# Kernel tuning notes

Measured on AMD Instinct MI355X. Metric: run time of the kernel, lower is better.

The kernel has to match this reference:

```python
import jax, jax.numpy as jnp
import numpy as np

U, S, D = 4096, 8192, 32
NUM_REGIONS = 128
GA = 0.1


def setup_inputs() -> dict:
    key = jax.random.key(0)
    k1, k2, k3, k4, k5, k6 = jax.random.split(key, 6)
    user_emb = jax.random.normal(k1, (U, D), dtype=jnp.float32) * 0.01
    item_emb = jax.random.normal(k2, (S, D), dtype=jnp.float32) * 0.01
    train_mask = jax.random.randint(k3, (U, S), 0, 2, dtype=jnp.int32)
    true_qos = jax.random.normal(k4, (U, S), dtype=jnp.float32)
    us_lossweight = jax.random.uniform(k5, (U, S), dtype=jnp.float32)
    region_index = jax.random.randint(k6, (U,), 0, NUM_REGIONS, dtype=jnp.int32)
    return {
        "user_emb": user_emb,
        "item_emb": item_emb,
        "train_mask": train_mask,
        "true_qos": true_qos,
        "us_lossweight": us_lossweight,
        "region_index": region_index,
    }


def _region_loss(user_emb, region_index):
    # per-region sums and counts via a single segment reduction
    sums = jax.ops.segment_sum(user_emb, region_index, num_segments=NUM_REGIONS)  # [R, D]
    counts = jax.ops.segment_sum(jnp.ones((user_emb.shape[0],), dtype=user_emb.dtype),
                                 region_index, num_segments=NUM_REGIONS)  # [R]
    cnt = counts[region_index]                      # [U]
    loo_mean = (sums[region_index] - user_emb) / jnp.maximum(cnt - 1.0, 1.0)[:, None]
    dev = jnp.abs(user_emb - loo_mean)              # [U, D]
    # regions with a single user are skipped in the original loop
    valid = (cnt > 1.0)[:, None]
    return jnp.sum(jnp.where(valid, dev, 0.0))


def reference(user_emb, item_emb, train_mask, true_qos, us_lossweight, region_index):
    pre_qos = (user_emb @ item_emb.T) * train_mask.astype(user_emb.dtype)  # [U, S]
    mse = (pre_qos - true_qos) ** 2
    loss = jnp.sum(us_lossweight * mse)
    regionloss = _region_loss(user_emb, region_index)
    return loss + GA * regionloss
```

## Files before the change

kernel.cpp:

```cpp
#include <hip/hip_runtime.h>

#define U 4096
#define S 8192
#define D 32
#define NUM_REGIONS 128
#define GA 0.1f

#define TU 32
#define TI 512
#define THREADS 256


__global__ void region_accum_kernel(const float* __restrict__ user_emb,
                                    const int* __restrict__ region_index,
                                    float* __restrict__ sums,
                                    float* __restrict__ counts) {
    int idx = blockIdx.x * blockDim.x + threadIdx.x;
    if (idx >= U * D) return;
    int u = idx >> 5;
    int d = idx & (D - 1);
    int r = region_index[u];
    atomicAdd(&sums[r * D + d], user_emb[idx]);
    if (d == 0) atomicAdd(&counts[r], 1.0f);
}

__global__ void region_loss_kernel(const float* __restrict__ user_emb,
                                   const int* __restrict__ region_index,
                                   const float* __restrict__ sums,
                                   const float* __restrict__ counts,
                                   float* __restrict__ rl_accum) {
    int idx = blockIdx.x * blockDim.x + threadIdx.x;
    float v = 0.0f;
    if (idx < U * D) {
        int u = idx >> 5;
        int d = idx & (D - 1);
        int r = region_index[u];
        float cnt = counts[r];
        if (cnt > 1.0f) {
            float e = user_emb[idx];
            float loo = (sums[r * D + d] - e) / fmaxf(cnt - 1.0f, 1.0f);
            v = fabsf(e - loo);
        }
    }
    #pragma unroll
    for (int off = 32; off > 0; off >>= 1) v += __shfl_down(v, off, 64);
    __shared__ float wp[THREADS / 64];
    int lane = threadIdx.x & 63, wid = threadIdx.x >> 6;
    if (lane == 0) wp[wid] = v;
    __syncthreads();
    if (threadIdx.x == 0) {
        float t = 0.0f;
        #pragma unroll
        for (int i = 0; i < THREADS / 64; i++) t += wp[i];
        atomicAdd(rl_accum, t);
    }
}


__global__ __launch_bounds__(THREADS) void mse_kernel(
    const float* __restrict__ user_emb,
    const float* __restrict__ item_emb,
    const int* __restrict__ train_mask,
    const float* __restrict__ true_qos,
    const float* __restrict__ us_lossweight,
    float* __restrict__ loss_accum) {
    __shared__ float uemb[TU][D];

    const int ub = blockIdx.x * TU;
    const int sb = blockIdx.y * TI;

    {
        const float4* src = (const float4*)(user_emb + (size_t)ub * D);
        ((float4*)&uemb[0][0])[threadIdx.x] = src[threadIdx.x];
    }
    __syncthreads();

    const int s0 = sb + 2 * threadIdx.x;

    float4 ir0[8], ir1[8];
    {
        const float4* ip0 = (const float4*)(item_emb + (size_t)s0 * D);
        const float4* ip1 = (const float4*)(item_emb + (size_t)(s0 + 1) * D);
        #pragma unroll
        for (int k = 0; k < 8; k++) { ir0[k] = ip0[k]; ir1[k] = ip1[k]; }
    }

    float acc = 0.0f;
    #pragma unroll 1
    for (int uu = 0; uu < TU; uu++) {
        const size_t base = (size_t)(ub + uu) * S + s0;
        int2   m = *(const int2*)(train_mask + base);
        float2 q = *(const float2*)(true_qos + base);
        float2 w = *(const float2*)(us_lossweight + base);

        float d0 = 0.0f, d1 = 0.0f;
        const float4* ur = (const float4*)&uemb[uu][0];
        #pragma unroll
        for (int k = 0; k < 8; k++) {
            float4 uv = ur[k];
            d0 += uv.x * ir0[k].x + uv.y * ir0[k].y + uv.z * ir0[k].z + uv.w * ir0[k].w;
            d1 += uv.x * ir1[k].x + uv.y * ir1[k].y + uv.z * ir1[k].z + uv.w * ir1[k].w;
        }
        float p0 = d0 * (float)m.x;
        float p1 = d1 * (float)m.y;
        float e0 = p0 - q.x;
        float e1 = p1 - q.y;
        acc += w.x * e0 * e0 + w.y * e1 * e1;
    }

    #pragma unroll
    for (int off = 32; off > 0; off >>= 1) acc += __shfl_down(acc, off, 64);
    __shared__ float wp[THREADS / 64];
    int lane = threadIdx.x & 63, wid = threadIdx.x >> 6;
    if (lane == 0) wp[wid] = acc;
    __syncthreads();
    if (threadIdx.x == 0) {
        float t = 0.0f;
        #pragma unroll
        for (int i = 0; i < THREADS / 64; i++) t += wp[i];
        atomicAdd(loss_accum, t);
    }
}

__global__ void finalize_kernel(const float* __restrict__ loss_acc,
                                const float* __restrict__ rl_acc,
                                float* __restrict__ out) {
    out[0] = loss_acc[0] + GA * rl_acc[0];
}

extern "C" void kernel_launch(void* const* d_in, const int* in_sizes, int n_in,
                              void* d_out, int out_size, void* d_ws, size_t ws_size,
                              hipStream_t stream) {
    const float* user_emb      = (const float*)d_in[0];
    const float* item_emb      = (const float*)d_in[1];
    const int*   train_mask    = (const int*)d_in[2];
    const float* true_qos      = (const float*)d_in[3];
    const float* us_lossweight = (const float*)d_in[4];
    const int*   region_index  = (const int*)d_in[5];
    float* out = (float*)d_out;

    float* ws       = (float*)d_ws;
    float* sums     = ws;
    float* counts   = sums + NUM_REGIONS * D;
    float* loss_acc = counts + NUM_REGIONS;
    float* rl_acc   = loss_acc + 1;
    size_t zero_bytes = (size_t)(NUM_REGIONS * D + NUM_REGIONS + 2) * sizeof(float);
    hipMemsetAsync(d_ws, 0, zero_bytes, stream);

    region_accum_kernel<<<(U * D + 255) / 256, 256, 0, stream>>>(
        user_emb, region_index, sums, counts);
    region_loss_kernel<<<(U * D + 255) / 256, 256, 0, stream>>>(
        user_emb, region_index, sums, counts, rl_acc);

    dim3 grid(U / TU, S / TI);
    mse_kernel<<<grid, THREADS, 0, stream>>>(
        user_emb, item_emb, train_mask, true_qos, us_lossweight, loss_acc);

    finalize_kernel<<<1, 1, 0, stream>>>(loss_acc, rl_acc, out);
}
```

Baseline: 401.8 us.

## Fuse region kernels per-region and prefetch next-row MSE inputs

Replaces the two atomic-based region kernels with a single kernel that has one block per region. Each block scans the region index held in shared memory and accumulates sums, counts and the leave-one-out loss without global atomics on sums. In the MSE kernel, the next user row's mask, target and weight values are software-prefetched, item registers are pinned with inline asm, and a min-blocks launch bound is added. The region kernel scans all users for every region, which adds redundant work, but that part is small next to the memory-bound MSE pass.

Measured after the change: 453.1 us. 1.13x slower.

```diff
diff --git a/kernel.cpp b/kernel.cpp
--- a/kernel.cpp
+++ b/kernel.cpp
@@ -11,53 +11,76 @@
 #define THREADS 256
 
 
-__global__ void region_accum_kernel(const float* __restrict__ user_emb,
-                                    const int* __restrict__ region_index,
-                                    float* __restrict__ sums,
-                                    float* __restrict__ counts) {
-    int idx = blockIdx.x * blockDim.x + threadIdx.x;
-    if (idx >= U * D) return;
-    int u = idx >> 5;
-    int d = idx & (D - 1);
-    int r = region_index[u];
-    atomicAdd(&sums[r * D + d], user_emb[idx]);
-    if (d == 0) atomicAdd(&counts[r], 1.0f);
-}
+__global__ __launch_bounds__(256) void region_kernel(
+    const float* __restrict__ user_emb,
+    const int* __restrict__ region_index,
+    float* __restrict__ rl_accum) {
+    __shared__ int   ridx[U];
+    __shared__ float part[8][D];
+    __shared__ float partc[8];
+    __shared__ float redsum[D];
+    __shared__ float redcnt;
 
-__global__ void region_loss_kernel(const float* __restrict__ user_emb,
-                                   const int* __restrict__ region_index,
-                                   const float* __restrict__ sums,
-                                   const float* __restrict__ counts,
-                                   float* __restrict__ rl_accum) {
-    int idx = blockIdx.x * blockDim.x + threadIdx.x;
-    float v = 0.0f;
-    if (idx < U * D) {
-        int u = idx >> 5;
-        int d = idx & (D - 1);
-        int r = region_index[u];
-        float cnt = counts[r];
-        if (cnt > 1.0f) {
-            float e = user_emb[idx];
-            float loo = (sums[r * D + d] - e) / fmaxf(cnt - 1.0f, 1.0f);
-            v = fabsf(e - loo);
+    for (int i = threadIdx.x; i < U / 4; i += 256)
+        ((int4*)ridx)[i] = ((const int4*)region_index)[i];
+    __syncthreads();
+
+    const int r = blockIdx.x;
+    const int d = threadIdx.x & (D - 1);
+    const int w = threadIdx.x >> 5;
+
+    float psum = 0.0f;
+    float pcnt = 0.0f;
+    for (int u = w; u < U; u += 8) {
+        if (ridx[u] == r) {
+            psum += user_emb[u * D + d];
+            pcnt += 1.0f;
         }
     }
+    part[w][d] = psum;
+    if (d == 0) partc[w] = pcnt;
+    __syncthreads();
+    if (w == 0) {
+        float s = 0.0f;
+        #pragma unroll
+        for (int i = 0; i < 8; i++) s += part[i][d];
+        redsum[d] = s;
+    }
+    if (threadIdx.x == 0) {
+        float c = 0.0f;
+        #pragma unroll
+        for (int i = 0; i < 8; i++) c += partc[i];
+        redcnt = c;
+    }
+    __syncthreads();
+
+    const float cnt = redcnt;
+    float acc = 0.0f;
+    if (cnt > 1.0f) {
+        const float inv = 1.0f / (cnt - 1.0f);
+        const float sd = redsum[d];
+        for (int u = w; u < U; u += 8) {
+            if (ridx[u] == r) {
+                float e = user_emb[u * D + d];
+                acc += fabsf(e - (sd - e) * inv);
+            }
+        }
+    }
+
     #pragma unroll
-    for (int off = 32; off > 0; off >>= 1) v += __shfl_down(v, off, 64);
-    __shared__ float wp[THREADS / 64];
+    for (int off = 32; off > 0; off >>= 1) acc += __shfl_down(acc, off, 64);
+    __shared__ float wp[4];
     int lane = threadIdx.x & 63, wid = threadIdx.x >> 6;
-    if (lane == 0) wp[wid] = v;
+    if (lane == 0) wp[wid] = acc;
     __syncthreads();
-    if (threadIdx.x == 0) {
-        float t = 0.0f;
-        #pragma unroll
-        for (int i = 0; i < THREADS / 64; i++) t += wp[i];
-        atomicAdd(rl_accum, t);
-    }
+    if (threadIdx.x == 0)
+        atomicAdd(rl_accum, wp[0] + wp[1] + wp[2] + wp[3]);
 }
 
 
-__global__ __launch_bounds__(THREADS) void mse_kernel(
+#define PIN4(v) asm volatile("" : "+v"(v.x), "+v"(v.y), "+v"(v.z), "+v"(v.w))
+
+__global__ __launch_bounds__(THREADS, 2) void mse_kernel(
     const float* __restrict__ user_emb,
     const float* __restrict__ item_emb,
     const int* __restrict__ train_mask,
@@ -73,7 +96,6 @@
         const float4* src = (const float4*)(user_emb + (size_t)ub * D);
         ((float4*)&uemb[0][0])[threadIdx.x] = src[threadIdx.x];
     }
-    __syncthreads();
 
     const int s0 = sb + 2 * threadIdx.x;
 
@@ -83,15 +105,28 @@
         const float4* ip1 = (const float4*)(item_emb + (size_t)(s0 + 1) * D);
         #pragma unroll
         for (int k = 0; k < 8; k++) { ir0[k] = ip0[k]; ir1[k] = ip1[k]; }
+        #pragma unroll
+        for (int k = 0; k < 8; k++) { PIN4(ir0[k]); PIN4(ir1[k]); }
     }
+    __syncthreads();
+
+    const size_t base0 = (size_t)ub * S + s0;
+    int2   m_n = *(const int2*)(train_mask + base0);
+    float2 q_n = *(const float2*)(true_qos + base0);
+    float2 w_n = *(const float2*)(us_lossweight + base0);
 
     float acc = 0.0f;
     #pragma unroll 1
     for (int uu = 0; uu < TU; uu++) {
-        const size_t base = (size_t)(ub + uu) * S + s0;
-        int2   m = *(const int2*)(train_mask + base);
-        float2 q = *(const float2*)(true_qos + base);
-        float2 w = *(const float2*)(us_lossweight + base);
+        int2   m = m_n;
+        float2 q = q_n;
+        float2 w = w_n;
+        if (uu + 1 < TU) {
+            const size_t nb = base0 + (size_t)(uu + 1) * S;
+            m_n = *(const int2*)(train_mask + nb);
+            q_n = *(const float2*)(true_qos + nb);
+            w_n = *(const float2*)(us_lossweight + nb);
+        }
 
         float d0 = 0.0f, d1 = 0.0f;
         const float4* ur = (const float4*)&uemb[uu][0];
@@ -140,17 +175,11 @@
     float* out = (float*)d_out;
 
     float* ws       = (float*)d_ws;
-    float* sums     = ws;
-    float* counts   = sums + NUM_REGIONS * D;
-    float* loss_acc = counts + NUM_REGIONS;
-    float* rl_acc   = loss_acc + 1;
-    size_t zero_bytes = (size_t)(NUM_REGIONS * D + NUM_REGIONS + 2) * sizeof(float);
-    hipMemsetAsync(d_ws, 0, zero_bytes, stream);
+    float* loss_acc = ws;
+    float* rl_acc   = ws + 1;
+    hipMemsetAsync(d_ws, 0, 2 * sizeof(float), stream);
 
-    region_accum_kernel<<<(U * D + 255) / 256, 256, 0, stream>>>(
-        user_emb, region_index, sums, counts);
-    region_loss_kernel<<<(U * D + 255) / 256, 256, 0, stream>>>(
-        user_emb, region_index, sums, counts, rl_acc);
+    region_kernel<<<NUM_REGIONS, 256, 0, stream>>>(user_emb, region_index, rl_acc);
 
     dim3 grid(U / TU, S / TI);
     mse_kernel<<<grid, THREADS, 0, stream>>>(
```
